# Kernel optimization log

Measured on AMD Instinct MI355X. Metric: run time of the kernel, lower is better.

## Reference

```python
import jax, jax.numpy as jnp
import numpy as np

B, M, L, HID, H, LAYERS = 16, 128, 512, 256, 4, 2
DH = HID // H  # 64 = head dim, also kernel_param dim


def _ln(x, g, b, eps=1e-5):
    mu = jnp.mean(x, axis=-1, keepdims=True)
    var = jnp.mean((x - mu) ** 2, axis=-1, keepdims=True)
    return (x - mu) / jnp.sqrt(var + eps) * g + b


def setup_inputs() -> dict:
    key = jax.random.key(0)
    ks = jax.random.split(key, 24)
    s = 0.05
    return {
        "ct_t": jax.random.uniform(ks[0], (B, M), jnp.float32),
        "ts_t": jax.random.uniform(ks[1], (B, L), jnp.float32),
        "ct_emb": jax.random.normal(ks[2], (B, M, HID), jnp.float32),
        "ts_emb": jax.random.normal(ks[3], (B, L, HID), jnp.float32),
        "kernel_param": jax.random.normal(ks[4], (DH,), jnp.float32),
        "ct_W": jax.random.normal(ks[5], (HID, HID), jnp.float32) * s,
        "ct_b": jnp.zeros((HID,), jnp.float32),
        "fW0": jax.random.normal(ks[6], (HID, HID), jnp.float32) * s,
        "fb0": jnp.zeros((HID,), jnp.float32),
        "fW1": jax.random.normal(ks[7], (HID, HID), jnp.float32) * s,
        "fb1": jnp.zeros((HID,), jnp.float32),
        "fW2": jax.random.normal(ks[8], (HID, HID), jnp.float32) * s,
        "fb2": jnp.zeros((HID,), jnp.float32),
        "f_ln_g": jnp.ones((HID,), jnp.float32),
        "f_ln_b": jnp.zeros((HID,), jnp.float32),
        "Wqkv": jax.random.normal(ks[9], (LAYERS, 3 * HID, HID), jnp.float32) * s,
        "bqkv": jnp.zeros((LAYERS, 3 * HID), jnp.float32),
        "Wo": jax.random.normal(ks[10], (LAYERS, HID, HID), jnp.float32) * s,
        "bo": jnp.zeros((LAYERS, HID), jnp.float32),
        "W1": jax.random.normal(ks[11], (LAYERS, 2 * HID, HID), jnp.float32) * s,
        "b1": jnp.zeros((LAYERS, 2 * HID), jnp.float32),
        "W2": jax.random.normal(ks[12], (LAYERS, HID, 2 * HID), jnp.float32) * s,
        "b2": jnp.zeros((LAYERS, HID), jnp.float32),
        "ln1_g": jnp.ones((LAYERS, HID), jnp.float32),
        "ln1_b": jnp.zeros((LAYERS, HID), jnp.float32),
        "ln2_g": jnp.ones((LAYERS, HID), jnp.float32),
        "ln2_b": jnp.zeros((LAYERS, HID), jnp.float32),
        "pred_W": jax.random.normal(ks[13], (1, HID), jnp.float32) * s,
        "pred_b": jnp.zeros((1,), jnp.float32),
    }


def reference(ct_t, ts_t, ct_emb, ts_emb, kernel_param, ct_W, ct_b,
              fW0, fb0, fW1, fb1, fW2, fb2, f_ln_g, f_ln_b,
              Wqkv, bqkv, Wo, bo, W1, b1, W2, b2,
              ln1_g, ln1_b, ln2_g, ln2_b, pred_W, pred_b):
    # --- TN tokenizer: multi-scale RBF kernel temporal fusion ---
    alpha = jax.nn.softplus(kernel_param)                       # [DH]  log(1+exp(p))
    ct_e = (jnp.einsum('bmd,ed->bme', ct_emb, ct_W) + ct_b)     # [B,M,HID]
    ct_e = ct_e.reshape(B, M, H, DH)
    diff = ct_t[:, :, None] - ts_t[:, None, :]                  # [B,M,L]
    norm = (diff * diff)[..., None]                             # [B,M,L,1]
    outs = []
    for s in range(H):                                          # fixed small loop over scales
        z = (-float(s)) * alpha * norm                          # [B,M,L,DH]
        w = jax.nn.logsumexp(z, axis=3, keepdims=True)          # [B,M,L,1]
        sim = jnp.exp(z - w)                                    # normalized kernel sims
        outs.append(jnp.einsum('bmnd,bmd->bnd', sim, ct_e[:, :, s, :]))  # scatter over ts events
    temp = jnp.concatenate(outs, axis=-1)                       # [B,L,HID]
    # --- Fusion module ---
    aux = jax.nn.elu(temp @ fW0.T + fb0 + ts_emb @ fW1.T + fb1)
    x = _ln(aux @ fW2.T + fb2 + ts_emb, f_ln_g, f_ln_b)         # [B,L,HID]
    # --- Transformer encoder (post-LN, gelu, no dropout at eval) ---
    inv_sqrt = 1.0 / np.sqrt(DH).astype(np.float32)
    for l in range(LAYERS):
        qkv = x @ Wqkv[l].T + bqkv[l]                           # [B,L,3*HID]
        q, k, v = jnp.split(qkv, 3, axis=-1)
        def heads(t):
            return t.reshape(B, L, H, DH).transpose(0, 2, 1, 3)
        q, k, v = heads(q), heads(k), heads(v)
        att = jax.nn.softmax(jnp.einsum('bhqd,bhkd->bhqk', q, k) * inv_sqrt, axis=-1)
        o = jnp.einsum('bhqk,bhkd->bhqd', att, v).transpose(0, 2, 1, 3).reshape(B, L, HID)
        x = _ln(x + o @ Wo[l].T + bo[l], ln1_g[l], ln1_b[l])
        ff = jax.nn.gelu(x @ W1[l].T + b1[l], approximate=False) @ W2[l].T + b2[l]
        x = _ln(x + ff, ln2_g[l], ln2_b[l])
    return x @ pred_W.T + pred_b                                # [B,L,1]
```

## Files before the change

### kernel.cpp

```cpp
#include <hip/hip_runtime.h>
#include <hip/hip_bf16.h>
#include <cstddef>

#define Bsz 16
#define Msz 128
#define Lsz 512
#define HIDs 256

typedef __attribute__((ext_vector_type(4))) float f32x4;
typedef __attribute__((ext_vector_type(8))) __bf16 bf16x8;
typedef __attribute__((ext_vector_type(8))) unsigned short ushort8;

#define CHEB_K 12
#define PI_F 3.14159265358979323846f

static __device__ inline unsigned short f2bf(float f) {
    __hip_bfloat16 h = __float2bfloat16(f);
    return *(unsigned short*)&h;
}
static __device__ inline float bf2f(unsigned short u) {
    return __builtin_bit_cast(float, (unsigned)u << 16);
}
static __device__ inline void gload16(const ushort* g, ushort* l) {
    __builtin_amdgcn_global_load_lds(
        (const __attribute__((address_space(1))) void*)g,
        (__attribute__((address_space(3))) void*)l, 16, 0, 0);
}

__global__ __launch_bounds__(256) void cheb_kernel(
    const float* __restrict__ kp, float* __restrict__ clut, float* __restrict__ cD)
{
    __shared__ float costab[CHEB_K][32];
    __shared__ float xq[32];
    __shared__ float alph[64];
    const int t = threadIdx.x;
    if (t < 64) {
        float p = kp[t];
        alph[t] = fmaxf(p, 0.f) + log1pf(__expf(-fabsf(p)));
    }
    #pragma unroll
    for (int i = 0; i < 2; i++) {
        int idx = i * 256 + t;
        if (idx < CHEB_K * 32) {
            int k = idx >> 5, q = idx & 31;
            float th = (q + 0.5f) * (PI_F / 32.f);
            costab[k][q] = __cosf((float)k * th);
        }
    }
    if (t < 32) xq[t] = 0.5f * (1.f + __cosf((t + 0.5f) * (PI_F / 32.f)));
    __syncthreads();

    if (t >= 192) return;
    const int d = t & 63, s1 = t >> 6;
    const float u = (float)(s1 + 1) * alph[d];
    float f[32];
    #pragma unroll
    for (int q = 0; q < 32; q++) f[q] = __expf(-u * xq[q]);
    #pragma unroll
    for (int k = 0; k < CHEB_K; k++) {
        float sum = 0.f;
        #pragma unroll
        for (int q = 0; q < 32; q++) sum = fmaf(f[q], costab[k][q], sum);
        float c = sum * ((k == 0 ? 1.f : 2.f) / 32.f);
        clut[s1 * (CHEB_K * 64) + k * 64 + d] = c;
        float sr = c;
        #pragma unroll
        for (int o = 1; o <= 32; o <<= 1) sr += __shfl_xor(sr, o, 64);
        if (d == 0) cD[s1 * CHEB_K + k] = sr;
    }
}

__global__ __launch_bounds__(256) void prep_kernel(
    const float* __restrict__ ts_emb, const float* __restrict__ ct_emb,
    const float* __restrict__ ct_W, const float* __restrict__ fW0,
    const float* __restrict__ fW1, const float* __restrict__ fW2,
    const float* __restrict__ Wqkv, const float* __restrict__ Wo,
    const float* __restrict__ W1, const float* __restrict__ W2,
    ushort* __restrict__ Xcat, ushort* __restrict__ Wcat,
    ushort* __restrict__ cebin, ushort* __restrict__ wct,
    ushort* __restrict__ wf2, ushort* __restrict__ wqkv,
    ushort* __restrict__ wo, ushort* __restrict__ w1, ushort* __restrict__ w2,
    const float* __restrict__ ct_t, const float* __restrict__ ts_t,
    const float* __restrict__ cD, ushort* __restrict__ invW,
    const float* __restrict__ bqkv, float* __restrict__ bqs)
{
    const int bid = blockIdx.x;
    const int tid = threadIdx.x;

    if (bid < 1920) {
        const unsigned u = bid * 256u + tid;
        const float* src; ushort* dst; unsigned rel;
        float sc = 1.f;
        if (u < 262144u) {
            rel = u; src = ts_emb;
            dst = Xcat + ((size_t)(rel >> 5) * 512 + 256 + (rel & 31) * 8);
        } else if (u < 327680u) { rel = u - 262144u; src = ct_emb; dst = cebin + (size_t)rel * 8; }
        else if (u < 335872u) { rel = u - 327680u; src = ct_W; dst = wct + (size_t)rel * 8; }
        else if (u < 344064u) { rel = u - 335872u; src = fW0;
            dst = Wcat + ((size_t)(rel >> 5) * 512 + (rel & 31) * 8); }
        else if (u < 352256u) { rel = u - 344064u; src = fW1;
            dst = Wcat + ((size_t)(rel >> 5) * 512 + 256 + (rel & 31) * 8); }
        else if (u < 360448u) { rel = u - 352256u; src = fW2; dst = wf2 + (size_t)rel * 8; }
        else if (u < 409600u) { rel = u - 360448u; src = Wqkv; dst = wqkv + (size_t)rel * 8;
            if (((rel >> 5) % 768) < 256) sc = 0.125f; }
        else if (u < 425984u) { rel = u - 409600u; src = Wo;  dst = wo + (size_t)rel * 8; }
        else if (u < 458752u) { rel = u - 425984u; src = W1;  dst = w1 + (size_t)rel * 8; }
        else                  { rel = u - 458752u; src = W2;  dst = w2 + (size_t)rel * 8; }
        float4 a = ((const float4*)src)[(size_t)rel * 2];
        float4 b = ((const float4*)src)[(size_t)rel * 2 + 1];
        ushort8 o;
        o[0] = f2bf(a.x * sc); o[1] = f2bf(a.y * sc); o[2] = f2bf(a.z * sc); o[3] = f2bf(a.w * sc);
        o[4] = f2bf(b.x * sc); o[5] = f2bf(b.y * sc); o[6] = f2bf(b.z * sc); o[7] = f2bf(b.w * sc);
        *(ushort8*)dst = o;
    } else if (bid < 6016) {
        __shared__ float cd[3][CHEB_K];
        if (tid < 3 * CHEB_K) cd[tid / CHEB_K][tid % CHEB_K] = cD[tid];
        __syncthreads();

        const unsigned G = (bid - 1920) * 256u + tid;
        const int b = G >> 16;
        const int n = (G >> 7) & 511;
        const int m = G & 127;

        float x = ct_t[b * Msz + m] - ts_t[b * Lsz + n];
        x = x * x;
        const float xi = 2.f * x - 1.f;
        const float xi2 = 2.f * xi;

        float t0 = 1.f, t1 = xi;
        float a1 = cd[0][0] + cd[0][1] * xi;
        float a2 = cd[1][0] + cd[1][1] * xi;
        float a3 = cd[2][0] + cd[2][1] * xi;
        #pragma unroll
        for (int k = 2; k < CHEB_K; k++) {
            float tn = fmaf(xi2, t1, -t0);
            a1 = fmaf(cd[0][k], tn, a1);
            a2 = fmaf(cd[1][k], tn, a2);
            a3 = fmaf(cd[2][k], tn, a3);
            t0 = t1; t1 = tn;
        }
        const size_t base = ((size_t)b * 3 * Lsz + n) * Msz + m;
        invW[base]                         = f2bf(1.f / a1);
        invW[base + (size_t)Lsz * Msz]     = f2bf(1.f / a2);
        invW[base + (size_t)2 * Lsz * Msz] = f2bf(1.f / a3);
    } else {
        #pragma unroll
        for (int i = 0; i < 6; i++) {
            int idx = i * 256 + tid;
            int c = idx % 768;
            bqs[idx] = bqkv[idx] * ((c < 256) ? 0.125f : 1.f);
        }
    }
}

__global__ __launch_bounds__(256) void gemm_mfma_kernel(
    const ushort* __restrict__ X, const ushort* __restrict__ W,
    const float* __restrict__ bias, const float* __restrict__ bias2,
    ushort* __restrict__ Yb, int NR, int K, int OUT, int act)
{
    __shared__ ushort As[2][64 * 64];
    __shared__ ushort Bs[2][128 * 64];

    const int nbx = OUT >> 7;
    const int bx = blockIdx.x % nbx;
    const int by = blockIdx.x / nbx;
    const int r0 = by << 6, o0 = bx << 7;
    const int tid = threadIdx.x;
    const int w = tid >> 6;
    const int lane = tid & 63;
    const int wr = w >> 1, wc = w & 1;
    const int lr = lane & 15, lg = lane >> 4;

    const int grow = lane >> 3;
    const int gchunk = (lane & 7) ^ grow;

    unsigned aoff[2][2], boff[4][2];
    #pragma unroll
    for (int f = 0; f < 2; f++) {
        unsigned cc = (unsigned)((lg + 4 * f) ^ (lr & 7)) * 16u;
        #pragma unroll
        for (int m = 0; m < 2; m++)
            aoff[m][f] = (unsigned)(wr * 32 + m * 16 + lr) * 128u + cc;
        #pragma unroll
        for (int n = 0; n < 4; n++)
            boff[n][f] = (unsigned)(wc * 64 + n * 16 + lr) * 128u + cc;
    }

    f32x4 acc[2][4];
    #pragma unroll
    for (int m = 0; m < 2; m++)
        #pragma unroll
        for (int n = 0; n < 4; n++) acc[m][n] = (f32x4){0.f, 0.f, 0.f, 0.f};

    const int nk = K >> 6;

    auto stage = [&](int buf, int ks) {
        const int k0 = ks << 6;
        #pragma unroll
        for (int i = 0; i < 2; i++) {
            int row = w * 16 + i * 8 + grow;
            gload16(X + (size_t)(r0 + row) * K + k0 + gchunk * 8,
                    &As[buf][(w * 16 + i * 8) * 64]);
        }
        #pragma unroll
        for (int i = 0; i < 4; i++) {
            int row = w * 32 + i * 8 + grow;
            gload16(W + (size_t)(o0 + row) * K + k0 + gchunk * 8,
                    &Bs[buf][(w * 32 + i * 8) * 64]);
        }
    };

    stage(0, 0);
    __syncthreads();
    int cur = 0;
    for (int ks = 0; ks < nk; ks++) {
        if (ks + 1 < nk) stage(cur ^ 1, ks + 1);
        const char* Ab = (const char*)As[cur];
        const char* Bb = (const char*)Bs[cur];
        #pragma unroll
        for (int f = 0; f < 2; f++) {
            bf16x8 av[2], bv[4];
            #pragma unroll
            for (int m = 0; m < 2; m++)
                av[m] = *(const bf16x8*)(Ab + aoff[m][f]);
            #pragma unroll
            for (int n = 0; n < 4; n++)
                bv[n] = *(const bf16x8*)(Bb + boff[n][f]);
            #pragma unroll
            for (int m = 0; m < 2; m++)
                #pragma unroll
                for (int n = 0; n < 4; n++)
                    acc[m][n] = __builtin_amdgcn_mfma_f32_16x16x32_bf16(
                        av[m], bv[n], acc[m][n], 0, 0, 0);
        }
        __syncthreads();
        cur ^= 1;
    }

    const int ocol0 = o0 + wc * 64;
    float bn[4];
    #pragma unroll
    for (int n = 0; n < 4; n++) {
        int o = ocol0 + n * 16 + lr;
        bn[n] = bias[o] + (bias2 ? bias2[o] : 0.f);
    }

    #pragma unroll
    for (int m = 0; m < 2; m++) {
        #pragma unroll
        for (int p = 0; p < 4; p++) {
            int r = r0 + wr * 32 + m * 16 + 4 * lg + p;
            size_t rb = (size_t)r * OUT;
            #pragma unroll
            for (int n = 0; n < 4; n++) {
                int o = ocol0 + n * 16 + lr;
                float v = acc[m][n][p] + bn[n];
                if (act == 1)      v = (v > 0.f) ? v : (__expf(v) - 1.f);
                else if (act == 2) v = 0.5f * v * (1.f + erff(v * 0.70710678118654752f));
                Yb[rb + o] = f2bf(v);
            }
        }
    }
}

__global__ __launch_bounds__(512) void gemm_ln_kernel(
    const ushort* __restrict__ X, const ushort* __restrict__ W,
    const float* __restrict__ bias, const ushort* __restrict__ add,
    int addS, int addO,
    const float* __restrict__ lng, const float* __restrict__ lnb,
    ushort* __restrict__ Xb,
    const float* __restrict__ predW, const float* __restrict__ predb,
    float* __restrict__ pout, int K)
{
    __shared__ ushort As[2][32 * 64];
    __shared__ ushort Bs[2][256 * 64];
    __shared__ float redA[32][4];
    __shared__ float redB[32][4];

    const int r0 = blockIdx.x << 5;
    const int tid = threadIdx.x;
    const int w = tid >> 6;
    const int lane = tid & 63;
    const int lr = lane & 15, lg = lane >> 4;
    const int wg = w >> 2;
    const int ws = w & 3;
    const int grow = lane >> 3;
    const int gchunk = (lane & 7) ^ grow;

    unsigned aoff[2], boff[4][2];
    #pragma unroll
    for (int f = 0; f < 2; f++) {
        unsigned cc = (unsigned)((lg + 4 * f) ^ (lr & 7)) * 16u;
        aoff[f] = (unsigned)(wg * 16 + lr) * 128u + cc;
        #pragma unroll
        for (int n = 0; n < 4; n++)
            boff[n][f] = (unsigned)(ws * 64 + n * 16 + lr) * 128u + cc;
    }

    f32x4 acc[4];
    #pragma unroll
    for (int n = 0; n < 4; n++) acc[n] = (f32x4){0.f, 0.f, 0.f, 0.f};

    const int nk = K >> 6;

    auto stage = [&](int buf, int ks) {
        const int k0 = ks << 6;
        if (w < 4)
            gload16(X + (size_t)(r0 + w * 8 + grow) * K + k0 + gchunk * 8,
                    &As[buf][(w * 8) * 64]);
        #pragma unroll
        for (int i = 0; i < 4; i++) {
            gload16(W + (size_t)(w * 32 + i * 8 + grow) * K + k0 + gchunk * 8,
                    &Bs[buf][(w * 32 + i * 8) * 64]);
        }
    };

    stage(0, 0);
    __syncthreads();
    int cur = 0;
    for (int ks = 0; ks < nk; ks++) {
        if (ks + 1 < nk) stage(cur ^ 1, ks + 1);
        const char* Ab = (const char*)As[cur];
        const char* Bb = (const char*)Bs[cur];
        #pragma unroll
        for (int f = 0; f < 2; f++) {
            bf16x8 av = *(const bf16x8*)(Ab + aoff[f]);
            #pragma unroll
            for (int n = 0; n < 4; n++) {
                bf16x8 bv = *(const bf16x8*)(Bb + boff[n][f]);
                acc[n] = __builtin_amdgcn_mfma_f32_16x16x32_bf16(
                    av, bv, acc[n], 0, 0, 0);
            }
        }
        __syncthreads();
        cur ^= 1;
    }

    const int col0 = ws * 64;
    float bn[4], gv[4], bv2[4], pwv[4];
    #pragma unroll
    for (int n = 0; n < 4; n++) {
        int o = col0 + n * 16 + lr;
        bn[n] = bias[o];
        gv[n] = lng[o];
        bv2[n] = lnb[o];
        pwv[n] = predW ? predW[o] : 0.f;
    }
    #pragma unroll
    for (int p = 0; p < 4; p++) {
        size_t ra = (size_t)(r0 + wg * 16 + 4 * lg + p) * addS + addO;
        #pragma unroll
        for (int n = 0; n < 4; n++)
            acc[n][p] += bn[n] + bf2f(add[ra + col0 + n * 16 + lr]);
    }

    #pragma unroll
    for (int p = 0; p < 4; p++) {
        float s = acc[0][p] + acc[1][p] + acc[2][p] + acc[3][p];
        #pragma unroll
        for (int o = 1; o <= 8; o <<= 1) s += __shfl_xor(s, o);
        if (lr == 0) redA[wg * 16 + 4 * lg + p][ws] = s;
    }
    __syncthreads();
    float mu[4];
    #pragma unroll
    for (int p = 0; p < 4; p++) {
        int row = wg * 16 + 4 * lg + p;
        mu[p] = (redA[row][0] + redA[row][1] + redA[row][2] + redA[row][3]) * (1.f / 256.f);
    }

    #pragma unroll
    for (int p = 0; p < 4; p++) {
        float q = 0.f;
        #pragma unroll
        for (int n = 0; n < 4; n++) {
            float dl = acc[n][p] - mu[p];
            q = fmaf(dl, dl, q);
        }
        #pragma unroll
        for (int o = 1; o <= 8; o <<= 1) q += __shfl_xor(q, o);
        if (lr == 0) redB[wg * 16 + 4 * lg + p][ws] = q;
    }
    __syncthreads();

    #pragma unroll
    for (int p = 0; p < 4; p++) {
        int row = wg * 16 + 4 * lg + p;
        float var = (redB[row][0] + redB[row][1] + redB[row][2] + redB[row][3]) * (1.f / 256.f);
        float rsig = rsqrtf(var + 1e-5f);
        size_t rb = (size_t)(r0 + row) * 256;
        float pd = 0.f;
        #pragma unroll
        for (int n = 0; n < 4; n++) {
            int o = col0 + n * 16 + lr;
            float xn = (acc[n][p] - mu[p]) * rsig * gv[n] + bv2[n];
            if (Xb) Xb[rb + o] = f2bf(xn);
            pd = fmaf(xn, pwv[n], pd);
        }
        if (predW) {
            #pragma unroll
            for (int o = 1; o <= 8; o <<= 1) pd += __shfl_xor(pd, o);
            if (lr == 0) redA[row][ws] = pd;
        }
    }
    if (predW) {
        __syncthreads();
        if (tid < 32)
            pout[r0 + tid] = redA[tid][0] + redA[tid][1] + redA[tid][2]
                           + redA[tid][3] + predb[0];
    }
}

__global__ __launch_bounds__(256) void tokmix_kernel(
    const float* __restrict__ ct_t, const float* __restrict__ ts_t,
    const ushort* __restrict__ ceb, const ushort* __restrict__ invW,
    const float* __restrict__ clut, ushort* __restrict__ Xcat)
{
    const int bid = blockIdx.x;
    const int tid = threadIdx.x;

    if (bid < 384) {
        const int nt = bid & 7;
        const int s1 = (bid >> 3) % 3;
        const int b  = bid / 24;
        const int w = tid >> 6, lane = tid & 63, g = lane >> 4, r = lane & 15;

        __shared__ ushort ceT[64][136];
        __shared__ float  cl[CHEB_K][64];
        __shared__ float  cts[128];

        #pragma unroll
        for (int i = 0; i < 8; i++) {
            int idx = i * 256 + tid;
            int m = idx >> 4, d4 = (idx & 15) << 2;
            const ushort* gp = ceb + (((size_t)b * 128 + m) << 8) + (s1 + 1) * 64 + d4;
            ushort4 v = *(const ushort4*)gp;
            ceT[d4 + 0][m] = v.x; ceT[d4 + 1][m] = v.y;
            ceT[d4 + 2][m] = v.z; ceT[d4 + 3][m] = v.w;
        }
        #pragma unroll
        for (int i = 0; i < 3; i++) {
            int idx = i * 256 + tid;
            cl[idx >> 6][idx & 63] = clut[s1 * (CHEB_K * 64) + idx];
        }
        if (tid < 128) cts[tid] = ct_t[b * 128 + tid];
        __syncthreads();

        const int nrow = nt * 64 + w * 16 + r;
        const float tsn = ts_t[b * 512 + nrow];

        float xi2v[4][8], Ta[4][8], Tb[4][8];
        #pragma unroll
        for (int t4 = 0; t4 < 4; t4++) {
            int m0 = 8 * g + 32 * t4;
            ushort8 iv = *(const ushort8*)&invW[((((size_t)b * 3 + s1) * 512 + nrow) << 7) + m0];
            #pragma unroll
            for (int j = 0; j < 8; j++) {
                float dfx = cts[m0 + j] - tsn;
                float x = dfx * dfx;
                float xi = 2.f * x - 1.f;
                float w0 = bf2f(iv[j]);
                xi2v[t4][j] = 2.f * xi;
                Ta[t4][j] = w0;
                Tb[t4][j] = w0 * xi;
            }
        }

        bf16x8 cef[4][4];
        #pragma unroll
        for (int db = 0; db < 4; db++)
            #pragma unroll
            for (int t4 = 0; t4 < 4; t4++)
                cef[db][t4] = *(const bf16x8*)&ceT[db * 16 + r][8 * g + 32 * t4];

        f32x4 acc[4];
        #pragma unroll
        for (int db = 0; db < 4; db++) acc[db] = (f32x4){0.f, 0.f, 0.f, 0.f};

        #pragma unroll
        for (int k = 0; k < CHEB_K; k++) {
            if (k >= 2) {
                #pragma unroll
                for (int t4 = 0; t4 < 4; t4++)
                    #pragma unroll
                    for (int j = 0; j < 8; j++) {
                        if (k & 1) Tb[t4][j] = fmaf(xi2v[t4][j], Ta[t4][j], -Tb[t4][j]);
                        else       Ta[t4][j] = fmaf(xi2v[t4][j], Tb[t4][j], -Ta[t4][j]);
                    }
            }
            bf16x8 af[4];
            #pragma unroll
            for (int t4 = 0; t4 < 4; t4++) {
                ushort8 u;
                #pragma unroll
                for (int j = 0; j < 8; j++)
                    u[j] = f2bf((k & 1) ? Tb[t4][j] : Ta[t4][j]);
                af[t4] = __builtin_bit_cast(bf16x8, u);
            }
            #pragma unroll
            for (int db = 0; db < 4; db++) {
                f32x4 gk = (f32x4){0.f, 0.f, 0.f, 0.f};
                #pragma unroll
                for (int t4 = 0; t4 < 4; t4++)
                    gk = __builtin_amdgcn_mfma_f32_16x16x32_bf16(af[t4], cef[db][t4], gk, 0, 0, 0);
                float ck = cl[k][db * 16 + r];
                #pragma unroll
                for (int p = 0; p < 4; p++) acc[db][p] = fmaf(ck, gk[p], acc[db][p]);
            }
        }

        #pragma unroll
        for (int db = 0; db < 4; db++)
            #pragma unroll
            for (int p = 0; p < 4; p++) {
                int n_out = nt * 64 + w * 16 + 4 * g + p;
                Xcat[((size_t)b * 512 + n_out) * 512 + (s1 + 1) * 64 + db * 16 + r] =
                    f2bf(acc[db][p]);
            }
    } else {
        const int b = bid - 384;
        const int d = tid & 63, q = tid >> 6;
        float s = 0.f;
        #pragma unroll 8
        for (int i = 0; i < 32; i++) {
            int m = q * 32 + i;
            s += bf2f(ceb[(((size_t)b * 128 + m) << 8) + d]);
        }
        __shared__ float red0[4][64];
        __shared__ ushort row0[64];
        red0[q][d] = s;
        __syncthreads();
        if (tid < 64)
            row0[tid] = f2bf((red0[0][tid] + red0[1][tid] + red0[2][tid] + red0[3][tid])
                             * (1.f / 64.f));
        __syncthreads();
        #pragma unroll
        for (int i = 0; i < 16; i++) {
            int idx = i * 256 + tid;
            int n = idx >> 3, j = idx & 7;
            *(ushort8*)&Xcat[((size_t)b * 512 + n) * 512 + j * 8] =
                *(const ushort8*)&row0[j * 8];
        }
    }
}

__global__ __launch_bounds__(256) void attn_mfma_kernel(
    const ushort* __restrict__ qkv, ushort* __restrict__ Ob)
{
    const int bid = blockIdx.x;
    const int qt = bid & 7;
    const int h  = (bid >> 3) & 3;
    const int b  = bid >> 5;
    const int t  = threadIdx.x;
    const int w  = t >> 6;
    const int lane = t & 63;
    const int g = lane >> 4;
    const int r = lane & 15;

    __shared__ ushort Ks[128][72];
    __shared__ ushort Vt[64][136];
    __shared__ float  Ps[4][16][129];

    const ushort* base = qkv + (size_t)b * Lsz * 768;
    const int q0 = qt * 64 + w * 16;

    bf16x8 qf[2];
    {
        const ushort* qp = base + (size_t)(q0 + r) * 768 + h * 64 + 8 * g;
        qf[0] = __builtin_bit_cast(bf16x8, *(const ushort8*)qp);
        qf[1] = __builtin_bit_cast(bf16x8, *(const ushort8*)(qp + 32));
    }

    f32x4 Ofr[4];
    #pragma unroll
    for (int dblk = 0; dblk < 4; dblk++) Ofr[dblk] = (f32x4){0.f, 0.f, 0.f, 0.f};
    float m_run[4] = {-1e30f, -1e30f, -1e30f, -1e30f};
    float l_run[4] = {0.f, 0.f, 0.f, 0.f};

    const int srow = t >> 1;
    const int sseg = t & 1;

    ushort8 pk[4], pv[4];
    auto gload_chunk = [&](int c) {
        const ushort* kr = base + (size_t)(c * 128 + srow) * 768 + 256 + h * 64 + sseg * 32;
        #pragma unroll
        for (int i = 0; i < 4; i++) {
            pk[i] = *(const ushort8*)(kr + 8 * i);
            pv[i] = *(const ushort8*)(kr + 256 + 8 * i);
        }
    };
    auto write_chunk = [&]() {
        #pragma unroll
        for (int i = 0; i < 4; i++) {
            *(ushort8*)&Ks[srow][sseg * 32 + 8 * i] = pk[i];
            #pragma unroll
            for (int j = 0; j < 8; j++)
                Vt[sseg * 32 + 8 * i + j][srow] = pv[i][j];
        }
    };

    gload_chunk(0);
    write_chunk();
    __syncthreads();

    for (int c = 0; c < 4; c++) {
        if (c < 3) gload_chunk(c + 1);

        f32x4 sfr[8];
        __builtin_amdgcn_s_setprio(1);
        #pragma unroll
        for (int s = 0; s < 8; s++) {
            f32x4 a2 = (f32x4){0.f, 0.f, 0.f, 0.f};
            #pragma unroll
            for (int f = 0; f < 2; f++) {
                bf16x8 kf = *(const bf16x8*)&Ks[s * 16 + r][8 * g + 32 * f];
                a2 = __builtin_amdgcn_mfma_f32_16x16x32_bf16(qf[f], kf, a2, 0, 0, 0);
            }
            sfr[s] = a2;
        }
        __builtin_amdgcn_s_setprio(0);

        #pragma unroll
        for (int p = 0; p < 4; p++) {
            float rm = sfr[0][p];
            #pragma unroll
            for (int s = 1; s < 8; s++) rm = fmaxf(rm, sfr[s][p]);
            #pragma unroll
            for (int o = 1; o <= 8; o <<= 1) rm = fmaxf(rm, __shfl_xor(rm, o));
            float mnew = fmaxf(m_run[p], rm);
            float sc = __expf(m_run[p] - mnew);
            m_run[p] = mnew;
            float rs = 0.f;
            #pragma unroll
            for (int s = 0; s < 8; s++) {
                float pvx = __expf(sfr[s][p] - mnew);
                Ps[w][4 * g + p][s * 16 + r] = pvx;
                rs += pvx;
            }
            #pragma unroll
            for (int o = 1; o <= 8; o <<= 1) rs += __shfl_xor(rs, o);
            l_run[p] = l_run[p] * sc + rs;
            #pragma unroll
            for (int dblk = 0; dblk < 4; dblk++) Ofr[dblk][p] *= sc;
        }

        __asm__ volatile("s_waitcnt lgkmcnt(0)" ::: "memory");

        #pragma unroll
        for (int ks2 = 0; ks2 < 4; ks2++) {
            const float* pp = &Ps[w][r][8 * g + 32 * ks2];
            ushort8 ua;
            #pragma unroll
            for (int j = 0; j < 8; j++) ua[j] = f2bf(pp[j]);
            bf16x8 pa = __builtin_bit_cast(bf16x8, ua);
            __builtin_amdgcn_s_setprio(1);
            #pragma unroll
            for (int dblk = 0; dblk < 4; dblk++) {
                bf16x8 vb = *(const bf16x8*)&Vt[dblk * 16 + r][32 * ks2 + 8 * g];
                Ofr[dblk] = __builtin_amdgcn_mfma_f32_16x16x32_bf16(
                    pa, vb, Ofr[dblk], 0, 0, 0);
            }
            __builtin_amdgcn_s_setprio(0);
        }

        __syncthreads();
        if (c < 3) {
            write_chunk();
            __syncthreads();
        }
    }

    #pragma unroll
    for (int dblk = 0; dblk < 4; dblk++) {
        #pragma unroll
        for (int p = 0; p < 4; p++) {
            int row = q0 + 4 * g + p;
            Ob[(size_t)(b * Lsz + row) * HIDs + h * 64 + dblk * 16 + r] =
                f2bf(Ofr[dblk][p] / l_run[p]);
        }
    }
}

extern "C" void kernel_launch(void* const* d_in, const int* in_sizes, int n_in,
                              void* d_out, int out_size, void* d_ws, size_t ws_size,
                              hipStream_t stream)
{
    (void)in_sizes; (void)n_in; (void)out_size; (void)ws_size;

    const float* ct_t   = (const float*)d_in[0];
    const float* ts_t   = (const float*)d_in[1];
    const float* ct_emb = (const float*)d_in[2];
    const float* ts_emb = (const float*)d_in[3];
    const float* kp     = (const float*)d_in[4];
    const float* ct_W   = (const float*)d_in[5];
    const float* ct_b   = (const float*)d_in[6];
    const float* fW0    = (const float*)d_in[7];
    const float* fb0    = (const float*)d_in[8];
    const float* fW1    = (const float*)d_in[9];
    const float* fb1    = (const float*)d_in[10];
    const float* fW2    = (const float*)d_in[11];
    const float* fb2    = (const float*)d_in[12];
    const float* f_ln_g = (const float*)d_in[13];
    const float* f_ln_b = (const float*)d_in[14];
    const float* Wqkv   = (const float*)d_in[15];
    const float* bqkv   = (const float*)d_in[16];
    const float* Wo     = (const float*)d_in[17];
    const float* bo     = (const float*)d_in[18];
    const float* W1     = (const float*)d_in[19];
    const float* b1     = (const float*)d_in[20];
    const float* W2     = (const float*)d_in[21];
    const float* b2     = (const float*)d_in[22];
    const float* ln1_g  = (const float*)d_in[23];
    const float* ln1_b  = (const float*)d_in[24];
    const float* ln2_g  = (const float*)d_in[25];
    const float* ln2_b  = (const float*)d_in[26];
    const float* pred_W = (const float*)d_in[27];
    const float* pred_b = (const float*)d_in[28];

    ushort* wsb = (ushort*)d_ws;
    ushort* invW  = wsb;
    ushort* auxbf = wsb;
    ushort* qkvbf = wsb;
    ushort* ff1bf = wsb;
    ushort* Xcat  = wsb + 12582912;
    ushort* Wcat  = wsb + 16777216;
    ushort* cebin = wsb + 16908288;
    ushort* cebout= wsb + 17432576;
    ushort* wct   = wsb + 17956864;
    ushort* wf2   = wsb + 18022400;
    ushort* wqkv  = wsb + 18087936;
    ushort* wo    = wsb + 18481152;
    ushort* w1    = wsb + 18612224;
    ushort* w2    = wsb + 18874368;
    ushort* xbf   = wsb + 19136512;
    ushort* obf   = wsb + 21233664;
    float*  wsf   = (float*)d_ws;
    float*  clut  = wsf + 11665408;
    float*  cDp   = wsf + 11667712;
    float*  bqs   = wsf + 11667776;

    const int NRts = Bsz * Lsz;
    const int NRct = Bsz * Msz;
    auto grid = [](int nr, int out) { return dim3((unsigned)((nr >> 6) * (out >> 7))); };

    cheb_kernel<<<dim3(1), 256, 0, stream>>>(kp, clut, cDp);
    prep_kernel<<<dim3(1920 + 4096 + 1), 256, 0, stream>>>(
        ts_emb, ct_emb, ct_W, fW0, fW1, fW2, Wqkv, Wo, W1, W2,
        Xcat, Wcat, cebin, wct, wf2, wqkv, wo, w1, w2,
        ct_t, ts_t, cDp, invW, bqkv, bqs);

    gemm_mfma_kernel<<<grid(NRct, 256), 256, 0, stream>>>(
        cebin, wct, ct_b, nullptr, cebout, NRct, 256, 256, 0);
    tokmix_kernel<<<dim3(400), 256, 0, stream>>>(ct_t, ts_t, cebout, invW, clut, Xcat);

    gemm_mfma_kernel<<<grid(NRts, 256), 256, 0, stream>>>(
        Xcat, Wcat, fb0, fb1, auxbf, NRts, 512, 256, 1);
    gemm_ln_kernel<<<dim3(NRts / 32), 512, 0, stream>>>(
        auxbf, wf2, fb2, Xcat, 512, 256, f_ln_g, f_ln_b, xbf,
        nullptr, nullptr, nullptr, 256);

    for (int l = 0; l < 2; l++) {
        gemm_mfma_kernel<<<grid(NRts, 768), 256, 0, stream>>>(
            xbf, wqkv + (size_t)l * 196608, bqs + l * 768, nullptr,
            qkvbf, NRts, 256, 768, 0);
        attn_mfma_kernel<<<dim3(512), 256, 0, stream>>>(qkvbf, obf);
        gemm_ln_kernel<<<dim3(NRts / 32), 512, 0, stream>>>(
            obf, wo + (size_t)l * 65536, bo + l * 256, xbf, 256, 0,
            ln1_g + l * 256, ln1_b + l * 256, xbf,
            nullptr, nullptr, nullptr, 256);
        gemm_mfma_kernel<<<grid(NRts, 512), 256, 0, stream>>>(
            xbf, w1 + (size_t)l * 131072, b1 + l * 512, nullptr,
            ff1bf, NRts, 256, 512, 2);
        if (l == 0) {
            gemm_ln_kernel<<<dim3(NRts / 32), 512, 0, stream>>>(
                ff1bf, w2 + (size_t)l * 131072, b2 + l * 256, xbf, 256, 0,
                ln2_g + l * 256, ln2_b + l * 256, xbf,
                nullptr, nullptr, nullptr, 512);
        } else {
            gemm_ln_kernel<<<dim3(NRts / 32), 512, 0, stream>>>(
                ff1bf, w2 + (size_t)l * 131072, b2 + l * 256, xbf, 256, 0,
                ln2_g + l * 256, ln2_b + l * 256, nullptr,
                pred_W, pred_b, (float*)d_out, 512);
        }
    }
}
```

Before: 190.0 us.

## Fold Chebyshev setup into consumers, add 128x128 QKV GEMM, widen attention blocks

```diff
diff --git a/kernel.cpp b/kernel.cpp
--- a/kernel.cpp
+++ b/kernel.cpp
@@ -25,49 +25,6 @@
     __builtin_amdgcn_global_load_lds(
         (const __attribute__((address_space(1))) void*)g,
         (__attribute__((address_space(3))) void*)l, 16, 0, 0);
-}
-
-__global__ __launch_bounds__(256) void cheb_kernel(
-    const float* __restrict__ kp, float* __restrict__ clut, float* __restrict__ cD)
-{
-    __shared__ float costab[CHEB_K][32];
-    __shared__ float xq[32];
-    __shared__ float alph[64];
-    const int t = threadIdx.x;
-    if (t < 64) {
-        float p = kp[t];
-        alph[t] = fmaxf(p, 0.f) + log1pf(__expf(-fabsf(p)));
-    }
-    #pragma unroll
-    for (int i = 0; i < 2; i++) {
-        int idx = i * 256 + t;
-        if (idx < CHEB_K * 32) {
-            int k = idx >> 5, q = idx & 31;
-            float th = (q + 0.5f) * (PI_F / 32.f);
-            costab[k][q] = __cosf((float)k * th);
-        }
-    }
-    if (t < 32) xq[t] = 0.5f * (1.f + __cosf((t + 0.5f) * (PI_F / 32.f)));
-    __syncthreads();
-
-    if (t >= 192) return;
-    const int d = t & 63, s1 = t >> 6;
-    const float u = (float)(s1 + 1) * alph[d];
-    float f[32];
-    #pragma unroll
-    for (int q = 0; q < 32; q++) f[q] = __expf(-u * xq[q]);
-    #pragma unroll
-    for (int k = 0; k < CHEB_K; k++) {
-        float sum = 0.f;
-        #pragma unroll
-        for (int q = 0; q < 32; q++) sum = fmaf(f[q], costab[k][q], sum);
-        float c = sum * ((k == 0 ? 1.f : 2.f) / 32.f);
-        clut[s1 * (CHEB_K * 64) + k * 64 + d] = c;
-        float sr = c;
-        #pragma unroll
-        for (int o = 1; o <= 32; o <<= 1) sr += __shfl_xor(sr, o, 64);
-        if (d == 0) cD[s1 * CHEB_K + k] = sr;
-    }
 }
 
 __global__ __launch_bounds__(256) void prep_kernel(
@@ -81,7 +38,7 @@
     ushort* __restrict__ wf2, ushort* __restrict__ wqkv,
     ushort* __restrict__ wo, ushort* __restrict__ w1, ushort* __restrict__ w2,
     const float* __restrict__ ct_t, const float* __restrict__ ts_t,
-    const float* __restrict__ cD, ushort* __restrict__ invW,
+    const float* __restrict__ kp, ushort* __restrict__ invW,
     const float* __restrict__ bqkv, float* __restrict__ bqs)
 {
     const int bid = blockIdx.x;
@@ -114,7 +71,37 @@
         *(ushort8*)dst = o;
     } else if (bid < 6016) {
         __shared__ float cd[3][CHEB_K];
-        if (tid < 3 * CHEB_K) cd[tid / CHEB_K][tid % CHEB_K] = cD[tid];
+        __shared__ float costab[CHEB_K][32];
+        __shared__ float xq[32];
+        #pragma unroll
+        for (int i = 0; i < 2; i++) {
+            int idx = i * 256 + tid;
+            if (idx < CHEB_K * 32) {
+                int k = idx >> 5, q = idx & 31;
+                costab[k][q] = __cosf((float)k * ((q + 0.5f) * (PI_F / 32.f)));
+            }
+        }
+        if (tid < 32) xq[tid] = 0.5f * (1.f + __cosf((tid + 0.5f) * (PI_F / 32.f)));
+        __syncthreads();
+        if (tid < 192) {
+            const int d = tid & 63, s1 = tid >> 6;
+            float p = kp[d];
+            float a = fmaxf(p, 0.f) + log1pf(__expf(-fabsf(p)));
+            const float u = (float)(s1 + 1) * a;
+            float f[32];
+            #pragma unroll
+            for (int q = 0; q < 32; q++) f[q] = __expf(-u * xq[q]);
+            #pragma unroll
+            for (int k = 0; k < CHEB_K; k++) {
+                float sum = 0.f;
+                #pragma unroll
+                for (int q = 0; q < 32; q++) sum = fmaf(f[q], costab[k][q], sum);
+                float c = sum * ((k == 0 ? 1.f : 2.f) / 32.f);
+                #pragma unroll
+                for (int o = 1; o <= 32; o <<= 1) c += __shfl_xor(c, o, 64);
+                if (d == 0) cd[s1][k] = c;
+            }
+        }
         __syncthreads();
 
         const unsigned G = (bid - 1920) * 256u + tid;
@@ -259,6 +246,104 @@
                 else if (act == 2) v = 0.5f * v * (1.f + erff(v * 0.70710678118654752f));
                 Yb[rb + o] = f2bf(v);
             }
+        }
+    }
+}
+
+__global__ __launch_bounds__(512) void gemm_mfma512_kernel(
+    const ushort* __restrict__ X, const ushort* __restrict__ W,
+    const float* __restrict__ bias, ushort* __restrict__ Yb,
+    int NR, int K, int OUT)
+{
+    __shared__ ushort As[2][128 * 64];
+    __shared__ ushort Bs[2][128 * 64];
+
+    const int nbx = OUT >> 7;
+    const int bx = blockIdx.x % nbx;
+    const int by = blockIdx.x / nbx;
+    const int r0 = by << 7, o0 = bx << 7;
+    const int tid = threadIdx.x;
+    const int w = tid >> 6;
+    const int lane = tid & 63;
+    const int wr = w >> 1, wc = w & 1;
+    const int lr = lane & 15, lg = lane >> 4;
+
+    const int grow = lane >> 3;
+    const int gchunk = (lane & 7) ^ grow;
+
+    unsigned aoff[2][2], boff[4][2];
+    #pragma unroll
+    for (int f = 0; f < 2; f++) {
+        unsigned cc = (unsigned)((lg + 4 * f) ^ (lr & 7)) * 16u;
+        #pragma unroll
+        for (int m = 0; m < 2; m++)
+            aoff[m][f] = (unsigned)(wr * 32 + m * 16 + lr) * 128u + cc;
+        #pragma unroll
+        for (int n = 0; n < 4; n++)
+            boff[n][f] = (unsigned)(wc * 64 + n * 16 + lr) * 128u + cc;
+    }
+
+    f32x4 acc[2][4];
+    #pragma unroll
+    for (int m = 0; m < 2; m++)
+        #pragma unroll
+        for (int n = 0; n < 4; n++) acc[m][n] = (f32x4){0.f, 0.f, 0.f, 0.f};
+
+    const int nk = K >> 6;
+
+    auto stage = [&](int buf, int ks) {
+        const int k0 = ks << 6;
+        #pragma unroll
+        for (int i = 0; i < 2; i++) {
+            int row = w * 16 + i * 8 + grow;
+            gload16(X + (size_t)(r0 + row) * K + k0 + gchunk * 8,
+                    &As[buf][(w * 16 + i * 8) * 64]);
+            gload16(W + (size_t)(o0 + row) * K + k0 + gchunk * 8,
+                    &Bs[buf][(w * 16 + i * 8) * 64]);
+        }
+    };
+
+    stage(0, 0);
+    __syncthreads();
+    int cur = 0;
+    for (int ks = 0; ks < nk; ks++) {
+        if (ks + 1 < nk) stage(cur ^ 1, ks + 1);
+        const char* Ab = (const char*)As[cur];
+        const char* Bb = (const char*)Bs[cur];
+        #pragma unroll
+        for (int f = 0; f < 2; f++) {
+            bf16x8 av[2], bv[4];
+            #pragma unroll
+            for (int m = 0; m < 2; m++)
+                av[m] = *(const bf16x8*)(Ab + aoff[m][f]);
+            #pragma unroll
+            for (int n = 0; n < 4; n++)
+                bv[n] = *(const bf16x8*)(Bb + boff[n][f]);
+            #pragma unroll
+            for (int m = 0; m < 2; m++)
+                #pragma unroll
+                for (int n = 0; n < 4; n++)
+                    acc[m][n] = __builtin_amdgcn_mfma_f32_16x16x32_bf16(
+                        av[m], bv[n], acc[m][n], 0, 0, 0);
+        }
+        __syncthreads();
+        cur ^= 1;
+    }
+
+    const int ocol0 = o0 + wc * 64;
+    float bn[4];
+    #pragma unroll
+    for (int n = 0; n < 4; n++) bn[n] = bias[ocol0 + n * 16 + lr];
+
+    #pragma unroll
+    for (int m = 0; m < 2; m++) {
+        #pragma unroll
+        for (int p = 0; p < 4; p++) {
+            int r = r0 + wr * 32 + m * 16 + 4 * lg + p;
+            size_t rb = (size_t)r * OUT;
+            #pragma unroll
+            for (int n = 0; n < 4; n++)
+                Yb[rb + ocol0 + n * 16 + lr] = f2bf(acc[m][n][p] + bn[n]);
         }
     }
 }
@@ -414,7 +499,7 @@
 __global__ __launch_bounds__(256) void tokmix_kernel(
     const float* __restrict__ ct_t, const float* __restrict__ ts_t,
     const ushort* __restrict__ ceb, const ushort* __restrict__ invW,
-    const float* __restrict__ clut, ushort* __restrict__ Xcat)
+    const float* __restrict__ kp, ushort* __restrict__ Xcat)
 {
     const int bid = blockIdx.x;
     const int tid = threadIdx.x;
@@ -428,6 +513,8 @@
         __shared__ ushort ceT[64][136];
         __shared__ float  cl[CHEB_K][64];
         __shared__ float  cts[128];
+        __shared__ float  costab[CHEB_K][32];
+        __shared__ float  xq[32];
 
         #pragma unroll
         for (int i = 0; i < 8; i++) {
@@ -439,12 +526,32 @@
             ceT[d4 + 2][m] = v.z; ceT[d4 + 3][m] = v.w;
         }
         #pragma unroll
-        for (int i = 0; i < 3; i++) {
+        for (int i = 0; i < 2; i++) {
             int idx = i * 256 + tid;
-            cl[idx >> 6][idx & 63] = clut[s1 * (CHEB_K * 64) + idx];
-        }
+            if (idx < CHEB_K * 32) {
+                int k = idx >> 5, q = idx & 31;
+                costab[k][q] = __cosf((float)k * ((q + 0.5f) * (PI_F / 32.f)));
+            }
+        }
+        if (tid < 32) xq[tid] = 0.5f * (1.f + __cosf((tid + 0.5f) * (PI_F / 32.f)));
         if (tid < 128) cts[tid] = ct_t[b * 128 + tid];
         __syncthreads();
+
+        if (tid < 64) {
+            float p = kp[tid];
+            float a = fmaxf(p, 0.f) + log1pf(__expf(-fabsf(p)));
+            const float u = (float)(s1 + 1) * a;
+            float f[32];
+            #pragma unroll
+            for (int q = 0; q < 32; q++) f[q] = __expf(-u * xq[q]);
+            #pragma unroll
+            for (int k = 0; k < CHEB_K; k++) {
+                float sum = 0.f;
+                #pragma unroll
+                for (int q = 0; q < 32; q++) sum = fmaf(f[q], costab[k][q], sum);
+                cl[k][tid] = sum * ((k == 0 ? 1.f : 2.f) / 32.f);
+            }
+        }
 
         const int nrow = nt * 64 + w * 16 + r;
         const float tsn = ts_t[b * 512 + nrow];
@@ -472,6 +579,8 @@
             #pragma unroll
             for (int t4 = 0; t4 < 4; t4++)
                 cef[db][t4] = *(const bf16x8*)&ceT[db * 16 + r][8 * g + 32 * t4];
+
+        __syncthreads();
 
         f32x4 acc[4];
         #pragma unroll
@@ -544,13 +653,13 @@
     }
 }
 
-__global__ __launch_bounds__(256) void attn_mfma_kernel(
+__global__ __launch_bounds__(512) void attn_mfma_kernel(
     const ushort* __restrict__ qkv, ushort* __restrict__ Ob)
 {
     const int bid = blockIdx.x;
-    const int qt = bid & 7;
-    const int h  = (bid >> 3) & 3;
-    const int b  = bid >> 5;
+    const int qt = bid & 3;
+    const int h  = (bid >> 2) & 3;
+    const int b  = bid >> 4;
     const int t  = threadIdx.x;
     const int w  = t >> 6;
     const int lane = t & 63;
@@ -559,10 +668,10 @@
 
     __shared__ ushort Ks[128][72];
     __shared__ ushort Vt[64][136];
-    __shared__ float  Ps[4][16][129];
+    __shared__ float  Ps[8][16][129];
 
     const ushort* base = qkv + (size_t)b * Lsz * 768;
-    const int q0 = qt * 64 + w * 16;
+    const int q0 = qt * 128 + w * 16;
 
     bf16x8 qf[2];
     {
@@ -577,25 +686,24 @@
     float m_run[4] = {-1e30f, -1e30f, -1e30f, -1e30f};
     float l_run[4] = {0.f, 0.f, 0.f, 0.f};
 
-    const int srow = t >> 1;
-    const int sseg = t & 1;
-
-    ushort8 pk[4], pv[4];
+    const int srow = t >> 2;
+    const int sseg = t & 3;
+
+    ushort8 pk[2], pv[2];
     auto gload_chunk = [&](int c) {
-        const ushort* kr = base + (size_t)(c * 128 + srow) * 768 + 256 + h * 64 + sseg * 32;
-        #pragma unroll
-        for (int i = 0; i < 4; i++) {
-            pk[i] = *(const ushort8*)(kr + 8 * i);
-            pv[i] = *(const ushort8*)(kr + 256 + 8 * i);
-        }
+        const ushort* kr = base + (size_t)(c * 128 + srow) * 768 + 256 + h * 64 + sseg * 16;
+        pk[0] = *(const ushort8*)kr;
+        pk[1] = *(const ushort8*)(kr + 8);
+        pv[0] = *(const ushort8*)(kr + 256);
+        pv[1] = *(const ushort8*)(kr + 264);
     };
     auto write_chunk = [&]() {
-        #pragma unroll
-        for (int i = 0; i < 4; i++) {
-            *(ushort8*)&Ks[srow][sseg * 32 + 8 * i] = pk[i];
-            #pragma unroll
-            for (int j = 0; j < 8; j++)
-                Vt[sseg * 32 + 8 * i + j][srow] = pv[i][j];
+        *(ushort8*)&Ks[srow][sseg * 16]     = pk[0];
+        *(ushort8*)&Ks[srow][sseg * 16 + 8] = pk[1];
+        #pragma unroll
+        for (int j = 0; j < 8; j++) {
+            Vt[sseg * 16 + j][srow]     = pv[0][j];
+            Vt[sseg * 16 + 8 + j][srow] = pv[1][j];
         }
     };
 
@@ -735,23 +843,20 @@
     ushort* xbf   = wsb + 19136512;
     ushort* obf   = wsb + 21233664;
     float*  wsf   = (float*)d_ws;
-    float*  clut  = wsf + 11665408;
-    float*  cDp   = wsf + 11667712;
-    float*  bqs   = wsf + 11667776;
+    float*  bqs   = wsf + 11665408;
 
     const int NRts = Bsz * Lsz;
     const int NRct = Bsz * Msz;
     auto grid = [](int nr, int out) { return dim3((unsigned)((nr >> 6) * (out >> 7))); };
 
-    cheb_kernel<<<dim3(1), 256, 0, stream>>>(kp, clut, cDp);
     prep_kernel<<<dim3(1920 + 4096 + 1), 256, 0, stream>>>(
         ts_emb, ct_emb, ct_W, fW0, fW1, fW2, Wqkv, Wo, W1, W2,
         Xcat, Wcat, cebin, wct, wf2, wqkv, wo, w1, w2,
-        ct_t, ts_t, cDp, invW, bqkv, bqs);
+        ct_t, ts_t, kp, invW, bqkv, bqs);
 
     gemm_mfma_kernel<<<grid(NRct, 256), 256, 0, stream>>>(
         cebin, wct, ct_b, nullptr, cebout, NRct, 256, 256, 0);
-    tokmix_kernel<<<dim3(400), 256, 0, stream>>>(ct_t, ts_t, cebout, invW, clut, Xcat);
+    tokmix_kernel<<<dim3(400), 256, 0, stream>>>(ct_t, ts_t, cebout, invW, kp, Xcat);
 
     gemm_mfma_kernel<<<grid(NRts, 256), 256, 0, stream>>>(
         Xcat, Wcat, fb0, fb1, auxbf, NRts, 512, 256, 1);
@@ -760,10 +865,9 @@
         nullptr, nullptr, nullptr, 256);
 
     for (int l = 0; l < 2; l++) {
-        gemm_mfma_kernel<<<grid(NRts, 768), 256, 0, stream>>>(
-            xbf, wqkv + (size_t)l * 196608, bqs + l * 768, nullptr,
-            qkvbf, NRts, 256, 768, 0);
-        attn_mfma_kernel<<<dim3(512), 256, 0, stream>>>(qkvbf, obf);
+        gemm_mfma512_kernel<<<dim3((NRts >> 7) * 6), 512, 0, stream>>>(
+            xbf, wqkv + (size_t)l * 196608, bqs + l * 768, qkvbf, NRts, 256, 768);
+        attn_mfma_kernel<<<dim3(256), 512, 0, stream>>>(qkvbf, obf);
         gemm_ln_kernel<<<dim3(NRts / 32), 512, 0, stream>>>(
             obf, wo + (size_t)l * 65536, bo + l * 256, xbf, 256, 0,
             ln1_g + l * 256, ln1_b + l * 256, xbf,
```

Measured after the change: 201.9 us, median of 2. 6.2% more time.
